# Kernel optimization log

Hardware: AMD Instinct MI355X
Metric: run time of the kernel (lower is better)

The kernel has to match this reference:

```python
import jax, jax.numpy as jnp
import numpy as np

P0, P1, P2 = 0, 9, 95          # player, status
P3 = 103                        # player_info end / cards start
P4 = P3 + 13 * 740              # 9723, cards end / potions start
P5 = P4 + 43                    # 9766, relics start
P6 = P5 + 180                   # 9946, monsters start
P7 = P6 + 5 * 101               # 10451


def setup_inputs() -> dict:
    key = jax.random.key(0)
    ks = jax.random.split(key, 8)
    def lin(k, out_f, in_f):
        # torch.nn.Linear default init: U(-1/sqrt(in), 1/sqrt(in)), weight [out, in]
        bound = 1.0 / np.sqrt(in_f)
        return jax.random.uniform(k, (out_f, in_f), jnp.float32, -bound, bound)
    return {
        "battle": jax.random.normal(ks[0], (32768, P7), jnp.float32),
        "W_player": lin(ks[1], 4, 9),
        "W_status": lin(ks[2], 16, 86),
        "W_pinfo": lin(ks[3], 2, 8),
        "W_card": lin(ks[4], 32, 740),
        "W_potions": lin(ks[5], 8, 43),
        "W_relics": lin(ks[6], 16, 180),
        "W_monster": lin(ks[7], 16, 101),
    }


def reference(battle, W_player, W_status, W_pinfo, W_card, W_potions, W_relics, W_monster):
    B = battle.shape[0]
    player = battle[:, P0:P1] @ W_player.T                     # [B, 4]
    status = battle[:, P1:P2] @ W_status.T                     # [B, 16]
    pinfo = battle[:, P2:P3] @ W_pinfo.T                       # [B, 2]
    # 13 card segments share one weight -> single batched GEMM
    cards = battle[:, P3:P4].reshape(B, 13, 740)
    cards = jnp.einsum('bsf,of->bso', cards, W_card).reshape(B, 13 * 32)
    potions = battle[:, P4:P5] @ W_potions.T                   # [B, 8]
    relics = battle[:, P5:P6] @ W_relics.T                     # [B, 16]
    # 5 monster segments share one weight
    monsters = battle[:, P6:P7].reshape(B, 5, 101)
    monsters = jnp.einsum('bsf,of->bso', monsters, W_monster).reshape(B, 5 * 16)
    # concat in the module's ModuleList order
    return jnp.concatenate([player, status, pinfo, cards, potions, relics, monsters], axis=-1)
```

## Files before the change

kernel.cpp:

```cpp
#include <hip/hip_runtime.h>
#include <stdint.h>


typedef __attribute__((ext_vector_type(8))) short short8;
typedef __attribute__((ext_vector_type(4))) float f32x4;

__device__ inline unsigned short f2bf(float f) {
  union { float f; uint32_t u; } v; v.f = f;
  uint32_t r = v.u + 0x7FFFu + ((v.u >> 16) & 1u);
  return (unsigned short)(r >> 16);
}

__device__ inline void gload_dw(const float* g, float* lds) {
  __builtin_amdgcn_global_load_lds(
      (const __attribute__((address_space(1))) void*)g,
      (__attribute__((address_space(3))) void*)lds, 4, 0, 0);
}

__global__ __launch_bounds__(256, 4) void seg_gemm(
    const float* __restrict__ battle,
    const float* __restrict__ Wplayer, const float* __restrict__ Wstatus,
    const float* __restrict__ Wpinfo,  const float* __restrict__ Wcard,
    const float* __restrict__ Wpotions,const float* __restrict__ Wrelics,
    const float* __restrict__ Wmonster,
    float* __restrict__ out, const float* __restrict__ zpage)
{
  const int bid = blockIdx.x;
  int bloc, nsub, K, NOUT, soff, ooff;
  const float* wp;
  if (bid < 3328)      { bloc = bid;        nsub = 13; K = 740; NOUT = 32; soff = 103;  ooff = 22;  wp = Wcard; }
  else if (bid < 4608) { bloc = bid - 3328; nsub = 5;  K = 101; NOUT = 16; soff = 9946; ooff = 462; wp = Wmonster; }
  else if (bid < 4864) { bloc = bid - 4608; nsub = 1;  K = 180; NOUT = 16; soff = 9766; ooff = 446; wp = Wrelics; }
  else if (bid < 5120) { bloc = bid - 4864; nsub = 1;  K = 86;  NOUT = 16; soff = 9;    ooff = 4;   wp = Wstatus; }
  else if (bid < 5376) { bloc = bid - 5120; nsub = 1;  K = 43;  NOUT = 8;  soff = 9723; ooff = 438; wp = Wpotions; }
  else if (bid < 5632) { bloc = bid - 5376; nsub = 1;  K = 9;   NOUT = 4;  soff = 0;    ooff = 0;   wp = Wplayer; }
  else                 { bloc = bid - 5632; nsub = 1;  K = 8;   NOUT = 2;  soff = 95;   ooff = 20;  wp = Wpinfo; }

  const int t    = threadIdx.x;
  const int lane = t & 63;
  const int wv   = t >> 6;
  const int rl   = lane & 15;
  const int kg   = lane >> 4;

  __shared__ float lds_a[128 * 32];
  __shared__ float lds_w[32 * 32];

  const int mb = bloc * 128;
  const int r0 = t >> 5;

  uint32_t rb[16];
  #pragma unroll
  for (int i = 0; i < 16; ++i) {
    uint32_t m   = (uint32_t)(mb + r0 + 8 * i);
    uint32_t b   = m / (uint32_t)nsub;
    uint32_t sub = m - b * (uint32_t)nsub;
    rb[i] = b * 10451u + (uint32_t)soff + sub * (uint32_t)K;
  }

  const int klin = t & 31;
  const int lk   = (((klin >> 2) ^ r0) << 2) | (klin & 3);

  f32x4 acc[2][2] = {};
  const int nfc = (NOUT > 16) ? 2 : 1;
  const int nch = (K + 31) >> 5;

  for (int ch = 0; ch < nch; ++ch) {
    const int k0 = ch << 5;
    const int kk = k0 + lk;
    #pragma unroll
    for (int i = 0; i < 16; ++i) {
      const float* sp = (kk < K) ? (battle + rb[i] + kk) : zpage;
      gload_dw(sp, &lds_a[i * 256 + t]);
    }
    #pragma unroll
    for (int i = 0; i < 4; ++i) {
      const int col = r0 + 8 * i;
      const float* sp = (col < NOUT && kk < K) ? (wp + col * K + kk) : zpage;
      gload_dw(sp, &lds_w[i * 256 + t]);
    }
    __syncthreads();

    short8 af[2], bfr[2];
    #pragma unroll
    for (int mf = 0; mf < 2; ++mf) {
      const int r  = wv * 32 + mf * 16 + rl;
      const int g0 = (2 * kg) ^ (r & 7);
      const int g1 = (2 * kg + 1) ^ (r & 7);
      f32x4 lo = *(const f32x4*)&lds_a[r * 32 + g0 * 4];
      f32x4 hi = *(const f32x4*)&lds_a[r * 32 + g1 * 4];
      af[mf][0] = (short)f2bf(lo[0]); af[mf][1] = (short)f2bf(lo[1]);
      af[mf][2] = (short)f2bf(lo[2]); af[mf][3] = (short)f2bf(lo[3]);
      af[mf][4] = (short)f2bf(hi[0]); af[mf][5] = (short)f2bf(hi[1]);
      af[mf][6] = (short)f2bf(hi[2]); af[mf][7] = (short)f2bf(hi[3]);
    }
    #pragma unroll
    for (int nf = 0; nf < 2; ++nf) {
      if (nf < nfc) {
        const int c  = nf * 16 + rl;
        const int g0 = (2 * kg) ^ (c & 7);
        const int g1 = (2 * kg + 1) ^ (c & 7);
        f32x4 lo = *(const f32x4*)&lds_w[c * 32 + g0 * 4];
        f32x4 hi = *(const f32x4*)&lds_w[c * 32 + g1 * 4];
        bfr[nf][0] = (short)f2bf(lo[0]); bfr[nf][1] = (short)f2bf(lo[1]);
        bfr[nf][2] = (short)f2bf(lo[2]); bfr[nf][3] = (short)f2bf(lo[3]);
        bfr[nf][4] = (short)f2bf(hi[0]); bfr[nf][5] = (short)f2bf(hi[1]);
        bfr[nf][6] = (short)f2bf(hi[2]); bfr[nf][7] = (short)f2bf(hi[3]);
      }
    }
    #pragma unroll
    for (int mf = 0; mf < 2; ++mf)
      #pragma unroll
      for (int nf = 0; nf < 2; ++nf)
        if (nf < nfc)
          acc[mf][nf] = __builtin_amdgcn_mfma_f32_16x16x32_bf16(af[mf], bfr[nf], acc[mf][nf], 0, 0, 0);
    __syncthreads();
  }

  #pragma unroll
  for (int mf = 0; mf < 2; ++mf) {
    #pragma unroll
    for (int q = 0; q < 4; ++q) {
      uint32_t m   = (uint32_t)(mb + wv * 32 + mf * 16 + (lane >> 4) * 4 + q);
      uint32_t b   = m / (uint32_t)nsub;
      uint32_t sub = m - b * (uint32_t)nsub;
      uint32_t ob  = b * 542u + (uint32_t)ooff + sub * (uint32_t)NOUT;
      #pragma unroll
      for (int nf = 0; nf < 2; ++nf) {
        if (nf < nfc) {
          const int col = nf * 16 + rl;
          if (col < NOUT) out[ob + col] = acc[mf][nf][q];
        }
      }
    }
  }
}

extern "C" void kernel_launch(void* const* d_in, const int* in_sizes, int n_in,
                              void* d_out, int out_size, void* d_ws, size_t ws_size,
                              hipStream_t stream) {
  const float* battle   = (const float*)d_in[0];
  const float* Wplayer  = (const float*)d_in[1];
  const float* Wstatus  = (const float*)d_in[2];
  const float* Wpinfo   = (const float*)d_in[3];
  const float* Wcard    = (const float*)d_in[4];
  const float* Wpotions = (const float*)d_in[5];
  const float* Wrelics  = (const float*)d_in[6];
  const float* Wmonster = (const float*)d_in[7];
  float* out = (float*)d_out;
  const float* zpage = (const float*)d_ws;

  hipMemsetAsync(d_ws, 0, 256, stream);

  dim3 grid(5888), block(256);
  hipLaunchKernelGGL(seg_gemm, grid, block, 0, stream,
                     battle, Wplayer, Wstatus, Wpinfo, Wcard, Wpotions,
                     Wrelics, Wmonster, out, zpage);
}
```

Measured before the change: 339.4 us.

## Double-buffer LDS staging to overlap next K-chunk loads with MFMA compute

Splits the LDS tiles into two buffers and issues the global-to-LDS loads for the next K chunk before computing on the current one. Partial vmcnt waits let each wave wait only for the older chunk's loads, and plain barriers replace __syncthreads. This is meant to hide global load latency behind the bf16 conversion and MFMA work. In exchange it doubles LDS use, which may reduce occupancy, and correctness depends on the hand-counted vmcnt value of 20 matching the number of outstanding loads per chunk.

```diff
diff --git a/kernel.cpp b/kernel.cpp
--- a/kernel.cpp
+++ b/kernel.cpp
@@ -42,8 +42,8 @@
   const int rl   = lane & 15;
   const int kg   = lane >> 4;
 
-  __shared__ float lds_a[128 * 32];
-  __shared__ float lds_w[32 * 32];
+  __shared__ float lds_a[2][128 * 32];
+  __shared__ float lds_w[2][32 * 32];
 
   const int mb = bloc * 128;
   const int r0 = t >> 5;
@@ -64,21 +64,31 @@
   const int nfc = (NOUT > 16) ? 2 : 1;
   const int nch = (K + 31) >> 5;
 
-  for (int ch = 0; ch < nch; ++ch) {
-    const int k0 = ch << 5;
-    const int kk = k0 + lk;
+  auto stage = [&](int ch, int pb) {
+    const int kk = (ch << 5) + lk;
     #pragma unroll
     for (int i = 0; i < 16; ++i) {
       const float* sp = (kk < K) ? (battle + rb[i] + kk) : zpage;
-      gload_dw(sp, &lds_a[i * 256 + t]);
+      gload_dw(sp, &lds_a[pb][i * 256 + t]);
     }
     #pragma unroll
     for (int i = 0; i < 4; ++i) {
       const int col = r0 + 8 * i;
       const float* sp = (col < NOUT && kk < K) ? (wp + col * K + kk) : zpage;
-      gload_dw(sp, &lds_w[i * 256 + t]);
+      gload_dw(sp, &lds_w[pb][i * 256 + t]);
     }
-    __syncthreads();
+  };
+
+  stage(0, 0);
+
+  for (int ch = 0; ch < nch; ++ch) {
+    const int cur = ch & 1;
+    if (ch + 1 < nch) {
+      stage(ch + 1, cur ^ 1);
+      asm volatile("s_waitcnt vmcnt(20)\n\ts_barrier" ::: "memory");
+    } else {
+      asm volatile("s_waitcnt vmcnt(0)\n\ts_barrier" ::: "memory");
+    }
 
     short8 af[2], bfr[2];
     #pragma unroll
@@ -86,8 +96,8 @@
       const int r  = wv * 32 + mf * 16 + rl;
       const int g0 = (2 * kg) ^ (r & 7);
       const int g1 = (2 * kg + 1) ^ (r & 7);
-      f32x4 lo = *(const f32x4*)&lds_a[r * 32 + g0 * 4];
-      f32x4 hi = *(const f32x4*)&lds_a[r * 32 + g1 * 4];
+      f32x4 lo = *(const f32x4*)&lds_a[cur][r * 32 + g0 * 4];
+      f32x4 hi = *(const f32x4*)&lds_a[cur][r * 32 + g1 * 4];
       af[mf][0] = (short)f2bf(lo[0]); af[mf][1] = (short)f2bf(lo[1]);
       af[mf][2] = (short)f2bf(lo[2]); af[mf][3] = (short)f2bf(lo[3]);
       af[mf][4] = (short)f2bf(hi[0]); af[mf][5] = (short)f2bf(hi[1]);
@@ -99,8 +109,8 @@
         const int c  = nf * 16 + rl;
         const int g0 = (2 * kg) ^ (c & 7);
         const int g1 = (2 * kg + 1) ^ (c & 7);
-        f32x4 lo = *(const f32x4*)&lds_w[c * 32 + g0 * 4];
-        f32x4 hi = *(const f32x4*)&lds_w[c * 32 + g1 * 4];
+        f32x4 lo = *(const f32x4*)&lds_w[cur][c * 32 + g0 * 4];
+        f32x4 hi = *(const f32x4*)&lds_w[cur][c * 32 + g1 * 4];
         bfr[nf][0] = (short)f2bf(lo[0]); bfr[nf][1] = (short)f2bf(lo[1]);
         bfr[nf][2] = (short)f2bf(lo[2]); bfr[nf][3] = (short)f2bf(lo[3]);
         bfr[nf][4] = (short)f2bf(hi[0]); bfr[nf][5] = (short)f2bf(hi[1]);
@@ -113,7 +123,8 @@
       for (int nf = 0; nf < 2; ++nf)
         if (nf < nfc)
           acc[mf][nf] = __builtin_amdgcn_mfma_f32_16x16x32_bf16(af[mf], bfr[nf], acc[mf][nf], 0, 0, 0);
-    __syncthreads();
+
+    asm volatile("s_barrier" ::: "memory");
   }
 
   #pragma unroll
@@ -139,8 +150,8 @@
                               void* d_out, int out_size, void* d_ws, size_t ws_size,
                               hipStream_t stream) {
   const float* battle   = (const float*)d_in[0];
+  const float* Wstatus  = (const float*)d_in[2];
   const float* Wplayer  = (const float*)d_in[1];
-  const float* Wstatus  = (const float*)d_in[2];
   const float* Wpinfo   = (const float*)d_in[3];
   const float* Wcard    = (const float*)d_in[4];
   const float* Wpotions = (const float*)d_in[5];
```

Result: no change. 339.7 us (+0.1%).

## Prepack bf16 padded weights and stream activations directly into registers

Applied to the files above, without the earlier changes.

Adds a small pre-kernel that converts all weight matrices to bf16, zero-padded to multiples of 128 in K, in workspace. The main kernel drops LDS staging and barriers. It loads activation rows straight into registers as unaligned float4 in 128-wide K chunks, relying on the zero-padded weights to cancel reads that spill into neighbouring segments. This cuts shared-memory traffic, synchronisation and per-block weight conversion, at the cost of an extra launch, some over-reading of activations and less regular global access.

```diff
diff --git a/kernel.cpp b/kernel.cpp
--- a/kernel.cpp
+++ b/kernel.cpp
@@ -4,6 +4,9 @@
 
 typedef __attribute__((ext_vector_type(8))) short short8;
 typedef __attribute__((ext_vector_type(4))) float f32x4;
+typedef __attribute__((ext_vector_type(4), aligned(4))) float f32x4u;
+
+#define TOTAL_ELS (32768u * 10451u)
 
 __device__ inline unsigned short f2bf(float f) {
   union { float f; uint32_t u; } v; v.f = f;
@@ -11,116 +14,117 @@
   return (unsigned short)(r >> 16);
 }
 
-__device__ inline void gload_dw(const float* g, float* lds) {
-  __builtin_amdgcn_global_load_lds(
-      (const __attribute__((address_space(1))) void*)g,
-      (__attribute__((address_space(3))) void*)lds, 4, 0, 0);
+__global__ __launch_bounds__(256) void pack_w(
+    const float* __restrict__ Wp, const float* __restrict__ Ws,
+    const float* __restrict__ Wpi, const float* __restrict__ Wc,
+    const float* __restrict__ Wpo, const float* __restrict__ Wr,
+    const float* __restrict__ Wm, unsigned short* __restrict__ wout)
+{
+  int el = blockIdx.x * 256 + threadIdx.x;
+  if (el >= 38912) return;
+  const float* w; int NOUT, K, Kp, woff;
+  if (el < 2048)       { w = Wp;  NOUT = 4;  K = 9;   Kp = 128; woff = 0; }
+  else if (el < 4096)  { w = Ws;  NOUT = 16; K = 86;  Kp = 128; woff = 2048; }
+  else if (el < 6144)  { w = Wpi; NOUT = 2;  K = 8;   Kp = 128; woff = 4096; }
+  else if (el < 30720) { w = Wc;  NOUT = 32; K = 740; Kp = 768; woff = 6144; }
+  else if (el < 32768) { w = Wpo; NOUT = 8;  K = 43;  Kp = 128; woff = 30720; }
+  else if (el < 36864) { w = Wr;  NOUT = 16; K = 180; Kp = 256; woff = 32768; }
+  else                 { w = Wm;  NOUT = 16; K = 101; Kp = 128; woff = 36864; }
+  int rel = el - woff;
+  int col = rel / Kp;
+  int k   = rel - col * Kp;
+  float v = (col < NOUT && k < K) ? w[col * K + k] : 0.0f;
+  wout[el] = f2bf(v);
 }
 
-__global__ __launch_bounds__(256, 4) void seg_gemm(
+__global__ __launch_bounds__(256, 3) void seg_gemm(
     const float* __restrict__ battle,
-    const float* __restrict__ Wplayer, const float* __restrict__ Wstatus,
-    const float* __restrict__ Wpinfo,  const float* __restrict__ Wcard,
-    const float* __restrict__ Wpotions,const float* __restrict__ Wrelics,
-    const float* __restrict__ Wmonster,
+    const unsigned short* __restrict__ wpack,
     float* __restrict__ out, const float* __restrict__ zpage)
 {
   const int bid = blockIdx.x;
-  int bloc, nsub, K, NOUT, soff, ooff;
-  const float* wp;
-  if (bid < 3328)      { bloc = bid;        nsub = 13; K = 740; NOUT = 32; soff = 103;  ooff = 22;  wp = Wcard; }
-  else if (bid < 4608) { bloc = bid - 3328; nsub = 5;  K = 101; NOUT = 16; soff = 9946; ooff = 462; wp = Wmonster; }
-  else if (bid < 4864) { bloc = bid - 4608; nsub = 1;  K = 180; NOUT = 16; soff = 9766; ooff = 446; wp = Wrelics; }
-  else if (bid < 5120) { bloc = bid - 4864; nsub = 1;  K = 86;  NOUT = 16; soff = 9;    ooff = 4;   wp = Wstatus; }
-  else if (bid < 5376) { bloc = bid - 5120; nsub = 1;  K = 43;  NOUT = 8;  soff = 9723; ooff = 438; wp = Wpotions; }
-  else if (bid < 5632) { bloc = bid - 5376; nsub = 1;  K = 9;   NOUT = 4;  soff = 0;    ooff = 0;   wp = Wplayer; }
-  else                 { bloc = bid - 5632; nsub = 1;  K = 8;   NOUT = 2;  soff = 95;   ooff = 20;  wp = Wpinfo; }
+  int bloc, nsub, K, NOUT, soff, ooff, Kp, woff;
+  if (bid < 3328)      { bloc = bid;        nsub = 13; K = 740; NOUT = 32; soff = 103;  ooff = 22;  Kp = 768; woff = 6144; }
+  else if (bid < 4608) { bloc = bid - 3328; nsub = 5;  K = 101; NOUT = 16; soff = 9946; ooff = 462; Kp = 128; woff = 36864; }
+  else if (bid < 4864) { bloc = bid - 4608; nsub = 1;  K = 180; NOUT = 16; soff = 9766; ooff = 446; Kp = 256; woff = 32768; }
+  else if (bid < 5120) { bloc = bid - 4864; nsub = 1;  K = 86;  NOUT = 16; soff = 9;    ooff = 4;   Kp = 128; woff = 2048; }
+  else if (bid < 5376) { bloc = bid - 5120; nsub = 1;  K = 43;  NOUT = 8;  soff = 9723; ooff = 438; Kp = 128; woff = 30720; }
+  else if (bid < 5632) { bloc = bid - 5376; nsub = 1;  K = 9;   NOUT = 4;  soff = 0;    ooff = 0;   Kp = 128; woff = 0; }
+  else                 { bloc = bid - 5632; nsub = 1;  K = 8;   NOUT = 2;  soff = 95;   ooff = 20;  Kp = 128; woff = 4096; }
 
   const int t    = threadIdx.x;
   const int lane = t & 63;
   const int wv   = t >> 6;
   const int rl   = lane & 15;
   const int kg   = lane >> 4;
+  const int mb   = bloc * 128 + wv * 32;
 
-  __shared__ float lds_a[128 * 32];
-  __shared__ float lds_w[32 * 32];
-
-  const int mb = bloc * 128;
-  const int r0 = t >> 5;
-
-  uint32_t rb[16];
+  uint32_t rb[2];
   #pragma unroll
-  for (int i = 0; i < 16; ++i) {
-    uint32_t m   = (uint32_t)(mb + r0 + 8 * i);
+  for (int mf = 0; mf < 2; ++mf) {
+    uint32_t m   = (uint32_t)(mb + mf * 16 + rl);
     uint32_t b   = m / (uint32_t)nsub;
     uint32_t sub = m - b * (uint32_t)nsub;
-    rb[i] = b * 10451u + (uint32_t)soff + sub * (uint32_t)K;
+    rb[mf] = b * 10451u + (uint32_t)soff + sub * (uint32_t)K;
   }
 
-  const int klin = t & 31;
-  const int lk   = (((klin >> 2) ^ r0) << 2) | (klin & 3);
+  const uint32_t LIM = TOTAL_ELS - 3u;
+  const int nfc = (NOUT > 16) ? 2 : 1;
+  const int nch = Kp >> 7;
+  const unsigned short* wbase = wpack + woff;
 
   f32x4 acc[2][2] = {};
-  const int nfc = (NOUT > 16) ? 2 : 1;
-  const int nch = (K + 31) >> 5;
 
   for (int ch = 0; ch < nch; ++ch) {
-    const int k0 = ch << 5;
-    const int kk = k0 + lk;
+    const uint32_t kb = (uint32_t)(ch * 128 + kg * 8);
+
+    f32x4 a[2][4][2];
     #pragma unroll
-    for (int i = 0; i < 16; ++i) {
-      const float* sp = (kk < K) ? (battle + rb[i] + kk) : zpage;
-      gload_dw(sp, &lds_a[i * 256 + t]);
-    }
-    #pragma unroll
-    for (int i = 0; i < 4; ++i) {
-      const int col = r0 + 8 * i;
-      const float* sp = (col < NOUT && kk < K) ? (wp + col * K + kk) : zpage;
-      gload_dw(sp, &lds_w[i * 256 + t]);
-    }
-    __syncthreads();
+    for (int mf = 0; mf < 2; ++mf)
+      #pragma unroll
+      for (int s = 0; s < 4; ++s)
+        #pragma unroll
+        for (int j = 0; j < 2; ++j) {
+          uint32_t g = rb[mf] + kb + (uint32_t)(s * 32 + j * 4);
+          const float* p = (g < LIM) ? (battle + g) : zpage;
+          a[mf][s][j] = *(const f32x4u*)p;
+        }
 
-    short8 af[2], bfr[2];
-    #pragma unroll
-    for (int mf = 0; mf < 2; ++mf) {
-      const int r  = wv * 32 + mf * 16 + rl;
-      const int g0 = (2 * kg) ^ (r & 7);
-      const int g1 = (2 * kg + 1) ^ (r & 7);
-      f32x4 lo = *(const f32x4*)&lds_a[r * 32 + g0 * 4];
-      f32x4 hi = *(const f32x4*)&lds_a[r * 32 + g1 * 4];
-      af[mf][0] = (short)f2bf(lo[0]); af[mf][1] = (short)f2bf(lo[1]);
-      af[mf][2] = (short)f2bf(lo[2]); af[mf][3] = (short)f2bf(lo[3]);
-      af[mf][4] = (short)f2bf(hi[0]); af[mf][5] = (short)f2bf(hi[1]);
-      af[mf][6] = (short)f2bf(hi[2]); af[mf][7] = (short)f2bf(hi[3]);
-    }
+    short8 wf[2][4];
     #pragma unroll
     for (int nf = 0; nf < 2; ++nf) {
       if (nf < nfc) {
-        const int c  = nf * 16 + rl;
-        const int g0 = (2 * kg) ^ (c & 7);
-        const int g1 = (2 * kg + 1) ^ (c & 7);
-        f32x4 lo = *(const f32x4*)&lds_w[c * 32 + g0 * 4];
-        f32x4 hi = *(const f32x4*)&lds_w[c * 32 + g1 * 4];
-        bfr[nf][0] = (short)f2bf(lo[0]); bfr[nf][1] = (short)f2bf(lo[1]);
-        bfr[nf][2] = (short)f2bf(lo[2]); bfr[nf][3] = (short)f2bf(lo[3]);
-        bfr[nf][4] = (short)f2bf(hi[0]); bfr[nf][5] = (short)f2bf(hi[1]);
-        bfr[nf][6] = (short)f2bf(hi[2]); bfr[nf][7] = (short)f2bf(hi[3]);
+        #pragma unroll
+        for (int s = 0; s < 4; ++s) {
+          const unsigned short* p = wbase + (uint32_t)((nf * 16 + rl) * Kp) + kb + (uint32_t)(s * 32);
+          wf[nf][s] = *(const short8*)p;
+        }
       }
     }
+
     #pragma unroll
-    for (int mf = 0; mf < 2; ++mf)
+    for (int s = 0; s < 4; ++s) {
       #pragma unroll
-      for (int nf = 0; nf < 2; ++nf)
-        if (nf < nfc)
-          acc[mf][nf] = __builtin_amdgcn_mfma_f32_16x16x32_bf16(af[mf], bfr[nf], acc[mf][nf], 0, 0, 0);
-    __syncthreads();
+      for (int mf = 0; mf < 2; ++mf) {
+        f32x4 lo = a[mf][s][0], hi = a[mf][s][1];
+        short8 aa;
+        aa[0] = (short)f2bf(lo[0]); aa[1] = (short)f2bf(lo[1]);
+        aa[2] = (short)f2bf(lo[2]); aa[3] = (short)f2bf(lo[3]);
+        aa[4] = (short)f2bf(hi[0]); aa[5] = (short)f2bf(hi[1]);
+        aa[6] = (short)f2bf(hi[2]); aa[7] = (short)f2bf(hi[3]);
+        #pragma unroll
+        for (int nf = 0; nf < 2; ++nf)
+          if (nf < nfc)
+            acc[mf][nf] = __builtin_amdgcn_mfma_f32_16x16x32_bf16(aa, wf[nf][s], acc[mf][nf], 0, 0, 0);
+      }
+    }
   }
 
   #pragma unroll
   for (int mf = 0; mf < 2; ++mf) {
     #pragma unroll
     for (int q = 0; q < 4; ++q) {
-      uint32_t m   = (uint32_t)(mb + wv * 32 + mf * 16 + (lane >> 4) * 4 + q);
+      uint32_t m   = (uint32_t)(mb + mf * 16 + kg * 4 + q);
       uint32_t b   = m / (uint32_t)nsub;
       uint32_t sub = m - b * (uint32_t)nsub;
       uint32_t ob  = b * 542u + (uint32_t)ooff + sub * (uint32_t)NOUT;
@@ -147,12 +151,14 @@
   const float* Wrelics  = (const float*)d_in[6];
   const float* Wmonster = (const float*)d_in[7];
   float* out = (float*)d_out;
+
   const float* zpage = (const float*)d_ws;
+  unsigned short* wpack = (unsigned short*)((char*)d_ws + 256);
 
   hipMemsetAsync(d_ws, 0, 256, stream);
-
-  dim3 grid(5888), block(256);
-  hipLaunchKernelGGL(seg_gemm, grid, block, 0, stream,
-                     battle, Wplayer, Wstatus, Wpinfo, Wcard, Wpotions,
-                     Wrelics, Wmonster, out, zpage);
+  hipLaunchKernelGGL(pack_w, dim3(152), dim3(256), 0, stream,
+                     Wplayer, Wstatus, Wpinfo, Wcard, Wpotions, Wrelics,
+                     Wmonster, wpack);
+  hipLaunchKernelGGL(seg_gemm, dim3(5888), dim3(256), 0, stream,
+                     battle, (const unsigned short*)wpack, out, zpage);
 }
```

Result: slower. 357.4 us (+5.3%).

## Restructure card GEMM: per-batch-row LDS staging with prepacked bf16 weights

Applied to the files above, without the earlier changes.

A small pre-kernel packs the shared card weight into bf16 MFMA fragment order. The card path then gets one block per two batch rows. Each block stages the 13x740 contiguous card span of both rows into LDS in a single pass and runs 24 MFMAs per wave without per-chunk syncs. Weight fragments are read straight from global memory instead of being converted from LDS. This is meant to remove the per-32-K chunk barriers, the redundant weight conversion and the row-index division overhead, at the cost of a much larger LDS footprint (about 76 KB), lower occupancy and an extra launch.

```diff
diff --git a/kernel.cpp b/kernel.cpp
--- a/kernel.cpp
+++ b/kernel.cpp
@@ -4,6 +4,8 @@
 
 typedef __attribute__((ext_vector_type(8))) short short8;
 typedef __attribute__((ext_vector_type(4))) float f32x4;
+
+#define TOTAL_ELS (32768u * 10451u)
 
 __device__ inline unsigned short f2bf(float f) {
   union { float f; uint32_t u; } v; v.f = f;
@@ -17,33 +19,95 @@
       (__attribute__((address_space(3))) void*)lds, 4, 0, 0);
 }
 
-__global__ __launch_bounds__(256, 4) void seg_gemm(
+__global__ __launch_bounds__(256) void pack_w(const float* __restrict__ Wc,
+                                              uint32_t* __restrict__ wout) {
+  int el = blockIdx.x * 256 + threadIdx.x;
+  if (el >= 12288) return;
+  int d  = el & 3;
+  int rl = (el >> 2) & 15;
+  int kg = (el >> 6) & 3;
+  int wn = (el >> 8) & 1;
+  int cs = el >> 9;
+  int s  = cs & 3, ch = cs >> 2;
+  int n  = wn * 16 + rl;
+  int k  = ch * 128 + s * 32 + kg * 8 + d * 2;
+  float v0 = (k     < 740) ? Wc[n * 740 + k]     : 0.0f;
+  float v1 = (k + 1 < 740) ? Wc[n * 740 + k + 1] : 0.0f;
+  wout[el] = (uint32_t)f2bf(v0) | ((uint32_t)f2bf(v1) << 16);
+}
+
+__global__ __launch_bounds__(256, 2) void seg_gemm(
     const float* __restrict__ battle,
     const float* __restrict__ Wplayer, const float* __restrict__ Wstatus,
-    const float* __restrict__ Wpinfo,  const float* __restrict__ Wcard,
-    const float* __restrict__ Wpotions,const float* __restrict__ Wrelics,
-    const float* __restrict__ Wmonster,
+    const float* __restrict__ Wpinfo,  const float* __restrict__ Wpotions,
+    const float* __restrict__ Wrelics, const float* __restrict__ Wmonster,
+    const uint32_t* __restrict__ wpack2,
     float* __restrict__ out, const float* __restrict__ zpage)
 {
+  __shared__ float shm[19456];
   const int bid = blockIdx.x;
-  int bloc, nsub, K, NOUT, soff, ooff;
-  const float* wp;
-  if (bid < 3328)      { bloc = bid;        nsub = 13; K = 740; NOUT = 32; soff = 103;  ooff = 22;  wp = Wcard; }
-  else if (bid < 4608) { bloc = bid - 3328; nsub = 5;  K = 101; NOUT = 16; soff = 9946; ooff = 462; wp = Wmonster; }
-  else if (bid < 4864) { bloc = bid - 4608; nsub = 1;  K = 180; NOUT = 16; soff = 9766; ooff = 446; wp = Wrelics; }
-  else if (bid < 5120) { bloc = bid - 4864; nsub = 1;  K = 86;  NOUT = 16; soff = 9;    ooff = 4;   wp = Wstatus; }
-  else if (bid < 5376) { bloc = bid - 5120; nsub = 1;  K = 43;  NOUT = 8;  soff = 9723; ooff = 438; wp = Wpotions; }
-  else if (bid < 5632) { bloc = bid - 5376; nsub = 1;  K = 9;   NOUT = 4;  soff = 0;    ooff = 0;   wp = Wplayer; }
-  else                 { bloc = bid - 5632; nsub = 1;  K = 8;   NOUT = 2;  soff = 95;   ooff = 20;  wp = Wpinfo; }
-
   const int t    = threadIdx.x;
   const int lane = t & 63;
   const int wv   = t >> 6;
   const int rl   = lane & 15;
   const int kg   = lane >> 4;
 
-  __shared__ float lds_a[128 * 32];
-  __shared__ float lds_w[32 * 32];
+  if (bid < 16384) {
+    const uint32_t g0 = (uint32_t)(bid * 2) * 10451u + 103u;
+    const uint32_t g1 = g0 + 10451u;
+    #pragma unroll
+    for (int r = 0; r < 38; ++r)
+      gload_dw(battle + g0 + (uint32_t)(r * 256 + t), &shm[r * 256 + t]);
+    #pragma unroll
+    for (int r = 0; r < 38; ++r)
+      gload_dw(battle + g1 + (uint32_t)(r * 256 + t), &shm[9728 + r * 256 + t]);
+    __syncthreads();
+
+    const int wm = wv >> 1;
+    const int wn = wv & 1;
+    const float* aspan = &shm[wm * 9728];
+    const uint32_t abase = (rl < 13) ? (uint32_t)(rl * 740) : 0u;
+
+    f32x4 acc = {0.f, 0.f, 0.f, 0.f};
+    for (int ch = 0; ch < 6; ++ch) {
+      #pragma unroll
+      for (int s = 0; s < 4; ++s) {
+        const float* ap = aspan + abase + (uint32_t)(ch * 128 + s * 32 + kg * 8);
+        f32x4 lo = *(const f32x4*)ap;
+        f32x4 hi = *(const f32x4*)(ap + 4);
+        short8 aa;
+        aa[0] = (short)f2bf(lo[0]); aa[1] = (short)f2bf(lo[1]);
+        aa[2] = (short)f2bf(lo[2]); aa[3] = (short)f2bf(lo[3]);
+        aa[4] = (short)f2bf(hi[0]); aa[5] = (short)f2bf(hi[1]);
+        aa[6] = (short)f2bf(hi[2]); aa[7] = (short)f2bf(hi[3]);
+        const int cs = ch * 4 + s;
+        short8 wf = *(const short8*)(wpack2 + (uint32_t)(cs * 512 + wn * 256 + kg * 64 + rl * 4));
+        acc = __builtin_amdgcn_mfma_f32_16x16x32_bf16(aa, wf, acc, 0, 0, 0);
+      }
+    }
+
+    const uint32_t b = (uint32_t)(bid * 2 + wm);
+    #pragma unroll
+    for (int q = 0; q < 4; ++q) {
+      const int sub = kg * 4 + q;
+      if (sub < 13)
+        out[b * 542u + 22u + (uint32_t)(sub * 32 + wn * 16 + rl)] = acc[q];
+    }
+    return;
+  }
+
+  const int sb = bid - 16384;
+  int bloc, nsub, K, NOUT, soff, ooff;
+  const float* wp;
+  if (sb < 1280)      { bloc = sb;        nsub = 5; K = 101; NOUT = 16; soff = 9946; ooff = 462; wp = Wmonster; }
+  else if (sb < 1536) { bloc = sb - 1280; nsub = 1; K = 180; NOUT = 16; soff = 9766; ooff = 446; wp = Wrelics; }
+  else if (sb < 1792) { bloc = sb - 1536; nsub = 1; K = 86;  NOUT = 16; soff = 9;    ooff = 4;   wp = Wstatus; }
+  else if (sb < 2048) { bloc = sb - 1792; nsub = 1; K = 43;  NOUT = 8;  soff = 9723; ooff = 438; wp = Wpotions; }
+  else if (sb < 2304) { bloc = sb - 2048; nsub = 1; K = 9;   NOUT = 4;  soff = 0;    ooff = 0;   wp = Wplayer; }
+  else                { bloc = sb - 2304; nsub = 1; K = 8;   NOUT = 2;  soff = 95;   ooff = 20;  wp = Wpinfo; }
+
+  float* lds_a = shm;
+  float* lds_w = shm + 4096;
 
   const int mb = bloc * 128;
   const int r0 = t >> 5;
@@ -60,13 +124,11 @@
   const int klin = t & 31;
   const int lk   = (((klin >> 2) ^ r0) << 2) | (klin & 3);
 
-  f32x4 acc[2][2] = {};
-  const int nfc = (NOUT > 16) ? 2 : 1;
+  f32x4 acc[2] = {};
   const int nch = (K + 31) >> 5;
 
   for (int ch = 0; ch < nch; ++ch) {
-    const int k0 = ch << 5;
-    const int kk = k0 + lk;
+    const int kk = (ch << 5) + lk;
     #pragma unroll
     for (int i = 0; i < 16; ++i) {
       const float* sp = (kk < K) ? (battle + rb[i] + kk) : zpage;
@@ -80,39 +142,34 @@
     }
     __syncthreads();
 
-    short8 af[2], bfr[2];
+    short8 af[2], bfr;
     #pragma unroll
     for (int mf = 0; mf < 2; ++mf) {
       const int r  = wv * 32 + mf * 16 + rl;
-      const int g0 = (2 * kg) ^ (r & 7);
-      const int g1 = (2 * kg + 1) ^ (r & 7);
-      f32x4 lo = *(const f32x4*)&lds_a[r * 32 + g0 * 4];
-      f32x4 hi = *(const f32x4*)&lds_a[r * 32 + g1 * 4];
+      const int g0i = (2 * kg) ^ (r & 7);
+      const int g1i = (2 * kg + 1) ^ (r & 7);
+      f32x4 lo = *(const f32x4*)&lds_a[r * 32 + g0i * 4];
+      f32x4 hi = *(const f32x4*)&lds_a[r * 32 + g1i * 4];
       af[mf][0] = (short)f2bf(lo[0]); af[mf][1] = (short)f2bf(lo[1]);
       af[mf][2] = (short)f2bf(lo[2]); af[mf][3] = (short)f2bf(lo[3]);
       af[mf][4] = (short)f2bf(hi[0]); af[mf][5] = (short)f2bf(hi[1]);
       af[mf][6] = (short)f2bf(hi[2]); af[mf][7] = (short)f2bf(hi[3]);
     }
-    #pragma unroll
-    for (int nf = 0; nf < 2; ++nf) {
-      if (nf < nfc) {
-        const int c  = nf * 16 + rl;
-        const int g0 = (2 * kg) ^ (c & 7);
-        const int g1 = (2 * kg + 1) ^ (c & 7);
-        f32x4 lo = *(const f32x4*)&lds_w[c * 32 + g0 * 4];
-        f32x4 hi = *(const f32x4*)&lds_w[c * 32 + g1 * 4];
-        bfr[nf][0] = (short)f2bf(lo[0]); bfr[nf][1] = (short)f2bf(lo[1]);
-        bfr[nf][2] = (short)f2bf(lo[2]); bfr[nf][3] = (short)f2bf(lo[3]);
-        bfr[nf][4] = (short)f2bf(hi[0]); bfr[nf][5] = (short)f2bf(hi[1]);
-        bfr[nf][6] = (short)f2bf(hi[2]); bfr[nf][7] = (short)f2bf(hi[3]);
-      }
+    {
+      const int c   = rl;
+      const int g0i = (2 * kg) ^ (c & 7);
+      const int g1i = (2 * kg + 1) ^ (c & 7);
+      f32x4 lo = *(const f32x4*)&lds_w[c * 32 + g0i * 4];
+      f32x4 hi = *(const f32x4*)&lds_w[c * 32 + g1i * 4];
+      bfr[0] = (short)f2bf(lo[0]); bfr[1] = (short)f2bf(lo[1]);
+      bfr[2] = (short)f2bf(lo[2]); bfr[3] = (short)f2bf(lo[3]);
+      bfr[4] = (short)f2bf(hi[0]); bfr[5] = (short)f2bf(hi[1]);
+      bfr[6] = (short)f2bf(hi[2]); bfr[7] = (short)f2bf(hi[3]);
     }
     #pragma unroll
     for (int mf = 0; mf < 2; ++mf)
-      #pragma unroll
-      for (int nf = 0; nf < 2; ++nf)
-        if (nf < nfc)
-          acc[mf][nf] = __builtin_amdgcn_mfma_f32_16x16x32_bf16(af[mf], bfr[nf], acc[mf][nf], 0, 0, 0);
+      acc[mf] = __builtin_amdgcn_mfma_f32_16x16x32_bf16(af[mf], bfr, acc[mf], 0, 0, 0);
+
     __syncthreads();
   }
 
@@ -120,17 +177,12 @@
   for (int mf = 0; mf < 2; ++mf) {
     #pragma unroll
     for (int q = 0; q < 4; ++q) {
-      uint32_t m   = (uint32_t)(mb + wv * 32 + mf * 16 + (lane >> 4) * 4 + q);
+      uint32_t m   = (uint32_t)(mb + wv * 32 + mf * 16 + kg * 4 + q);
       uint32_t b   = m / (uint32_t)nsub;
       uint32_t sub = m - b * (uint32_t)nsub;
       uint32_t ob  = b * 542u + (uint32_t)ooff + sub * (uint32_t)NOUT;
-      #pragma unroll
-      for (int nf = 0; nf < 2; ++nf) {
-        if (nf < nfc) {
-          const int col = nf * 16 + rl;
-          if (col < NOUT) out[ob + col] = acc[mf][nf][q];
-        }
-      }
+      const int col = rl;
+      if (col < NOUT) out[ob + col] = acc[mf][q];
     }
   }
 }
@@ -147,12 +199,13 @@
   const float* Wrelics  = (const float*)d_in[6];
   const float* Wmonster = (const float*)d_in[7];
   float* out = (float*)d_out;
+
   const float* zpage = (const float*)d_ws;
+  uint32_t* wpack2 = (uint32_t*)((char*)d_ws + 256);
 
   hipMemsetAsync(d_ws, 0, 256, stream);
-
-  dim3 grid(5888), block(256);
-  hipLaunchKernelGGL(seg_gemm, grid, block, 0, stream,
-                     battle, Wplayer, Wstatus, Wpinfo, Wcard, Wpotions,
-                     Wrelics, Wmonster, out, zpage);
-}
+  hipLaunchKernelGGL(pack_w, dim3(48), dim3(256), 0, stream, Wcard, wpack2);
+  hipLaunchKernelGGL(seg_gemm, dim3(18944), dim3(256), 0, stream,
+                     battle, Wplayer, Wstatus, Wpinfo, Wpotions, Wrelics,
+                     Wmonster, (const uint32_t*)wpack2, out, zpage);
+}
```

New measurement: 309.2 us. -8.9%, faster.
